# Performance work log

Measured on AMD Instinct MI355X. Metric: run time of the kernel, lower is better.

## Reference

```python
import jax, jax.numpy as jnp
import numpy as np


def _lstm_dir(xg, m, Whh, reverse):
    # xg: (T,B,4H) precomputed x@Wih.T + b ; m: (T,B) float mask
    T, B, G = xg.shape
    H = G // 4
    if reverse:
        xg = xg[::-1]
        m = m[::-1]

    def step(carry, inp):
        h, c = carry
        xg_t, m_t = inp
        gates = xg_t + h @ Whh.T
        i, f, g, o = jnp.split(gates, 4, axis=-1)  # torch gate order i,f,g,o
        i = jax.nn.sigmoid(i); f = jax.nn.sigmoid(f)
        g = jnp.tanh(g); o = jax.nn.sigmoid(o)
        c_new = f * c + i * g
        h_new = o * jnp.tanh(c_new)
        mt = m_t[:, None]
        h = mt * h_new + (1.0 - mt) * h
        c = mt * c_new + (1.0 - mt) * c
        return (h, c), h * mt  # zero outputs at padding like pad_packed_sequence

    init = (jnp.zeros((B, H), xg.dtype), jnp.zeros((B, H), xg.dtype))
    _, hs = jax.lax.scan(step, init, (xg, m))
    if reverse:
        hs = hs[::-1]
    return hs  # (T,B,H)


def _viterbi(feats, mask_f, transitions):
    # feats: (B,T,K) emissions incl. START/STOP rows; mask_f: (B,T) float
    B, T, K = feats.shape
    START, STOP = K - 2, K - 1
    part0 = transitions[START][None, :] + feats[:, 0, :]  # (B,K)
    ident = jnp.broadcast_to(jnp.arange(K)[None, :], (B, K))

    def step(part, inp):
        feat_t, m_t = inp
        cur = part[:, :, None] + transitions[None, :, :] + feat_t[:, None, :]
        new = cur.max(axis=1)
        bp = cur.argmax(axis=1)
        mb = (m_t > 0)[:, None]
        part = jnp.where(mb, new, part)        # carry partition through padding
        bp = jnp.where(mb, bp, ident)          # identity pointer at padding
        return part, bp

    part, bps = jax.lax.scan(
        step, part0, (feats[:, 1:].transpose(1, 0, 2), mask_f[:, 1:].T))
    final = part + transitions[:, STOP][None, :]
    best_score = final.max(axis=-1)            # (B,)
    last_tag = final.argmax(axis=-1)           # (B,)

    def back(tag, bp_t):
        prev = jnp.take_along_axis(bp_t, tag[:, None], axis=1)[:, 0]
        return prev, prev

    _, prevs = jax.lax.scan(back, last_tag, bps, reverse=True)  # (T-1,B)
    decode = jnp.concatenate([prevs, last_tag[None, :]], axis=0).T  # (B,T)
    return best_score, decode


def setup_inputs() -> dict:
    key = jax.random.key(0)
    ks = jax.random.split(key, 16)
    B, T, E, H = 256, 200, 256, 256
    Vc, Vf, n_labels = 10000, 100, 50
    K = n_labels + 2
    lengths = jnp.sort(jax.random.randint(ks[0], (B,), 1, T + 1))[::-1]
    lengths = lengths.at[0].set(T)
    mask = jnp.arange(T)[None, :] < lengths[:, None]
    s = 0.1
    trans = s * jax.random.normal(ks[11], (K, K), jnp.float32)
    trans = trans.at[:, K - 2].set(-10000.0)  # nothing transitions to START
    trans = trans.at[K - 1, :].set(-10000.0)  # nothing transitions from STOP
    return {
        'batch_input': jax.random.randint(ks[1], (B, T), 0, Vc),
        'batch_feature': jax.random.randint(ks[2], (B, T), 0, Vf),
        'batch_len': lengths,
        'batch_recover': jnp.arange(B),
        'mask': mask,
        'char_table': s * jax.random.normal(ks[3], (Vc, E), jnp.float32),
        'feat_table': 1.0 + s * jax.random.normal(ks[4], (Vf, E), jnp.float32),
        'Wih_f': s * jax.random.normal(ks[5], (4 * H, E), jnp.float32),
        'Whh_f': s * jax.random.normal(ks[6], (4 * H, H), jnp.float32),
        'b_f': s * jax.random.normal(ks[7], (4 * H,), jnp.float32),
        'Wih_b': s * jax.random.normal(ks[8], (4 * H, E), jnp.float32),
        'Whh_b': s * jax.random.normal(ks[9], (4 * H, H), jnp.float32),
        'b_b': s * jax.random.normal(ks[10], (4 * H,), jnp.float32),
        'W_tag': s * jax.random.normal(ks[12], (K, 2 * H), jnp.float32),
        'b_tag': s * jax.random.normal(ks[13], (K,), jnp.float32),
        'transitions': trans,
    }


def reference(batch_input, batch_feature, batch_len, batch_recover, mask,
              char_table, feat_table, Wih_f, Whh_f, b_f, Wih_b, Whh_b, b_b,
              W_tag, b_tag, transitions):
    # embeddings (dropout is identity at inference)
    emb = char_table[batch_input] * feat_table[batch_feature]  # (B,T,E)
    x = emb.transpose(1, 0, 2)                                 # (T,B,E)
    m = mask.astype(x.dtype).T                                 # (T,B)
    xg_f = jnp.einsum('tbe,ge->tbg', x, Wih_f) + b_f
    xg_b = jnp.einsum('tbe,ge->tbg', x, Wih_b) + b_b
    h_f = _lstm_dir(xg_f, m, Whh_f, reverse=False)
    h_b = _lstm_dir(xg_b, m, Whh_b, reverse=True)
    lstm_out = jnp.concatenate([h_f, h_b], axis=-1).transpose(1, 0, 2)  # (B,T,2H)
    feats = jnp.einsum('bth,kh->btk', lstm_out, W_tag) + b_tag          # (B,T,K)
    best_score, decode = _viterbi(feats, mask.astype(feats.dtype), transitions)
    decode = decode * mask.astype(decode.dtype)
    return best_score, decode
```

## Files before the change

kernel.cpp:

```cpp
#include <hip/hip_runtime.h>
#include <math.h>

#define T_ 200
#define WROW 284
#define SMEM_FLOATS (128 * WROW + 16 * WROW)
#define SMEM_BYTES (SMEM_FLOATS * 4)

typedef float f32x2 __attribute__((ext_vector_type(2)));

__device__ __forceinline__ float fsig(float x) {
  return 1.f / (1.f + __expf(-x));
}
__device__ __forceinline__ float ftanh(float x) {
  return 1.f - 2.f / (__expf(2.f * x) + 1.f);
}
__device__ __forceinline__ float dpp_xor1(float x) {
  return __int_as_float(__builtin_amdgcn_update_dpp(
      0, __float_as_int(x), 0xB1, 0xF, 0xF, true));
}
__device__ __forceinline__ float dpp_xor2(float x) {
  return __int_as_float(__builtin_amdgcn_update_dpp(
      0, __float_as_int(x), 0x4E, 0xF, 0xF, true));
}

__global__ __launch_bounds__(256) void xg_gemm(
    const int* __restrict__ bin, const int* __restrict__ bfe,
    const int* __restrict__ blen,
    const float* __restrict__ ctab, const float* __restrict__ ftab,
    const float* __restrict__ wihf, const float* __restrict__ biasf,
    const float* __restrict__ wihb, const float* __restrict__ biasb,
    float* __restrict__ xgf, float* __restrict__ xgb, int cc) {
  const int dir = blockIdx.z;
  const int m0 = blockIdx.x * 128;
  const int rloc = m0 >> 8;
  const int t_blk = dir ? (199 - cc - rloc) : (cc + rloc);
  if (t_blk >= blen[m0 & 255]) return;

  const float* wih  = dir ? wihb : wihf;
  const float* bias = dir ? biasb : biasf;
  float* xgslot     = dir ? xgb : xgf;

  __shared__ float As[32][140];
  __shared__ float Bs[32][132];
  const int tid = threadIdx.x;
  const int n0 = blockIdx.y * 128;
  const int mm = tid & 15;
  const int nn = tid >> 4;

  const int ra = tid & 127;
  const int ka = (tid >> 7) << 4;

  const int bcol = (m0 + ra) & 255;
  const float* cr = ctab + ((size_t)bin[bcol * T_ + t_blk] << 8);
  const float* fr = ftab + ((size_t)bfe[bcol * T_ + t_blk] << 8);
  const float* br = wih + (size_t)(n0 + ra) * 256;
  const int cwa = ra + ((ra >> 5) << 2);

  f32x2 acc[8][4];
  #pragma unroll
  for (int i = 0; i < 8; ++i)
    #pragma unroll
    for (int j = 0; j < 4; ++j) acc[i][j] = (f32x2){0.f, 0.f};

  const int am0 = mm * 8 + ((mm >> 2) << 2);
  const int bn0 = nn * 8;

  for (int ks = 0; ks < 256; ks += 32) {
    float4 c4[4], f4v[4], b4[4];
    #pragma unroll
    for (int w = 0; w < 4; ++w) {
      c4[w]  = *(const float4*)(cr + ks + ka + w * 4);
      f4v[w] = *(const float4*)(fr + ks + ka + w * 4);
      b4[w]  = *(const float4*)(br + ks + ka + w * 4);
    }
    __syncthreads();
    #pragma unroll
    for (int w = 0; w < 4; ++w) {
      int kk = ka + w * 4;
      As[kk + 0][cwa] = c4[w].x * f4v[w].x;
      As[kk + 1][cwa] = c4[w].y * f4v[w].y;
      As[kk + 2][cwa] = c4[w].z * f4v[w].z;
      As[kk + 3][cwa] = c4[w].w * f4v[w].w;
      Bs[kk + 0][ra] = b4[w].x;
      Bs[kk + 1][ra] = b4[w].y;
      Bs[kk + 2][ra] = b4[w].z;
      Bs[kk + 3][ra] = b4[w].w;
    }
    __syncthreads();
    #pragma unroll 4
    for (int k = 0; k < 32; ++k) {
      float4 a0 = *(const float4*)&As[k][am0];
      float4 a1 = *(const float4*)&As[k][am0 + 4];
      float4 b0 = *(const float4*)&Bs[k][bn0];
      float4 b1 = *(const float4*)&Bs[k][bn0 + 4];
      float am[8] = {a0.x, a0.y, a0.z, a0.w, a1.x, a1.y, a1.z, a1.w};
      f32x2 bp[4] = {{b0.x, b0.y}, {b0.z, b0.w}, {b1.x, b1.y}, {b1.z, b1.w}};
      #pragma unroll
      for (int i = 0; i < 8; ++i) {
        f32x2 av = {am[i], am[i]};
        #pragma unroll
        for (int j = 0; j < 4; ++j)
          acc[i][j] = __builtin_elementwise_fma(av, bp[j], acc[i][j]);
      }
    }
  }

  float4 bv0 = *(const float4*)(bias + n0 + bn0);
  float4 bv1 = *(const float4*)(bias + n0 + bn0 + 4);
  #pragma unroll
  for (int i = 0; i < 8; ++i) {
    int row = m0 + mm * 8 + i;
    float4 o0, o1;
    o0.x = acc[i][0].x + bv0.x; o0.y = acc[i][0].y + bv0.y;
    o0.z = acc[i][1].x + bv0.z; o0.w = acc[i][1].y + bv0.w;
    o1.x = acc[i][2].x + bv1.x; o1.y = acc[i][2].y + bv1.y;
    o1.z = acc[i][3].x + bv1.z; o1.w = acc[i][3].y + bv1.w;
    *(float4*)(xgslot + (size_t)row * 1024 + n0 + bn0) = o0;
    *(float4*)(xgslot + (size_t)row * 1024 + n0 + bn0 + 4) = o1;
  }
}

__global__ __launch_bounds__(512, 1) void lstm_chunk(
    const float* __restrict__ xgf, const float* __restrict__ xgb,
    const float* __restrict__ whf, const float* __restrict__ whb,
    const int* __restrict__ blen,
    float* __restrict__ hst, float* __restrict__ cst,
    float* __restrict__ hout, unsigned* __restrict__ bar,
    int s0, int nsteps) {
  extern __shared__ float smem[];
  float* wlds = smem;
  float* hlds = smem + 128 * WROW;

  const int bc = blockIdx.x, js = blockIdx.y, dir = blockIdx.z;
  const int tid = threadIdx.x;
  const int ks = tid & 7;
  const int bg = (tid >> 3) & 3;
  const int rg = tid >> 5;
  const int grp = dir * 16 + bc;
  const float* wh = dir ? whb : whf;
  const float* xgp = dir ? xgb : xgf;

  #pragma unroll
  for (int i = 0; i < 16; ++i) {
    int f = tid + i * 512;
    int prow = f >> 6;
    int k = (f & 63) << 2;
    int g = (prow >> 1) & 3, u = prow & 1, rgs = prow >> 3;
    int jg = js * 32 + rgs * 2 + u;
    float4 v = *(const float4*)(wh + ((size_t)(g * 256 + jg)) * 256 + k);
    *(float4*)&wlds[prow * WROW + k + ((k >> 5) << 2)] = v;
  }

  const int bl_th = bg * 4 + (ks & 3);
  const int b_th = bc * 16 + bl_th;
  const int u_th = ks >> 2;
  const int jth = js * 32 + rg * 2 + u_th;
  const int cjth = jth + ((jth >> 5) << 2);
  const int len_th = blen[b_th];
  float c0 = cst[((size_t)dir * 256 + b_th) * 256 + jth];

  float xq[4];
  #pragma unroll
  for (int g = 0; g < 4; ++g)
    xq[g] = xgp[(size_t)b_th * 1024 + g * 256 + jth];

  float hprev = 0.f;

  __syncthreads();

  for (int r = 0; r < nsteps; ++r) {
    const int s = s0 + r;
    const int tt = dir ? (199 - s) : s;
    const int rslot = s & 1, wslot = 1 - rslot;

    const float* hsrc = hst + (((size_t)(rslot * 2 + dir)) * 256 + bc * 16) * 256;
    {
      const int f0 = tid, f1 = tid + 512;
      const int b0i = f0 >> 6, k0 = (f0 & 63) << 2;
      const int b1i = f1 >> 6, k1 = (f1 & 63) << 2;
      const float* p0 = hsrc + (b0i << 8) + k0;
      const float* p1 = hsrc + (b1i << 8) + k1;
      float4 v0, v1;
      asm volatile(
          "global_load_dwordx4 %0, %2, off sc1\n\t"
          "global_load_dwordx4 %1, %3, off sc1\n\t"
          "s_waitcnt vmcnt(0)"
          : "=&v"(v0), "=&v"(v1)
          : "v"(p0), "v"(p1)
          : "memory");
      *(float4*)&hlds[b0i * WROW + k0 + ((k0 >> 5) << 2)] = v0;
      *(float4*)&hlds[b1i * WROW + k1 + ((k1 >> 5) << 2)] = v1;
    }
    __syncthreads();

    if (r == 0) hprev = hlds[bl_th * WROW + cjth];

    float xqn[4];
    const int rn = (r + 1 < nsteps) ? (r + 1) : r;
    #pragma unroll
    for (int g = 0; g < 4; ++g)
      xqn[g] = xgp[((size_t)rn * 256 + b_th) * 1024 + g * 256 + jth];

    f32x2 acc2[8][4];
    #pragma unroll
    for (int i = 0; i < 8; ++i)
      #pragma unroll
      for (int bb = 0; bb < 4; ++bb) acc2[i][bb] = (f32x2){0.f, 0.f};

    float4 w4c[8];
    #pragma unroll
    for (int i = 0; i < 8; ++i)
      w4c[i] = *(const float4*)&wlds[(rg * 8 + i) * WROW + ks * 36];

    #pragma unroll
    for (int kq = 0; kq < 8; ++kq) {
      const int col = ks * 36 + kq * 4;
      float4 h4[4];
      #pragma unroll
      for (int bb = 0; bb < 4; ++bb)
        h4[bb] = *(const float4*)&hlds[(bg * 4 + bb) * WROW + col];
      float4 w4n[8];
      if (kq < 7) {
        #pragma unroll
        for (int i = 0; i < 8; ++i)
          w4n[i] = *(const float4*)&wlds[(rg * 8 + i) * WROW + col + 4];
      }
      f32x2 hlo[4], hhi[4];
      #pragma unroll
      for (int bb = 0; bb < 4; ++bb) {
        hlo[bb] = (f32x2){h4[bb].x, h4[bb].y};
        hhi[bb] = (f32x2){h4[bb].z, h4[bb].w};
      }
      #pragma unroll
      for (int i = 0; i < 8; ++i) {
        f32x2 wlo = (f32x2){w4c[i].x, w4c[i].y};
        f32x2 whi = (f32x2){w4c[i].z, w4c[i].w};
        #pragma unroll
        for (int bb = 0; bb < 4; ++bb) {
          acc2[i][bb] = __builtin_elementwise_fma(wlo, hlo[bb], acc2[i][bb]);
          acc2[i][bb] = __builtin_elementwise_fma(whi, hhi[bb], acc2[i][bb]);
        }
      }
      if (kq < 7) {
        #pragma unroll
        for (int i = 0; i < 8; ++i) w4c[i] = w4n[i];
      }
    }

    float acc[8][4];
    #pragma unroll
    for (int i = 0; i < 8; ++i)
      #pragma unroll
      for (int bb = 0; bb < 4; ++bb)
        acc[i][bb] = acc2[i][bb].x + acc2[i][bb].y;

    const int bit0 = ks & 1, bit1 = (ks >> 1) & 1;
    float fin[8];
    #pragma unroll
    for (int i = 0; i < 8; ++i) {
      float k0 = bit0 ? acc[i][1] : acc[i][0];
      float s0v = bit0 ? acc[i][0] : acc[i][1];
      float k1 = bit0 ? acc[i][3] : acc[i][2];
      float s1v = bit0 ? acc[i][2] : acc[i][3];
      float r0 = k0 + dpp_xor1(s0v);
      float r1 = k1 + dpp_xor1(s1v);
      float k2 = bit1 ? r1 : r0;
      float s2v = bit1 ? r0 : r1;
      float r2 = k2 + dpp_xor2(s2v);
      fin[i] = r2 + __shfl_xor(r2, 4);
    }

    float gi = fsig((u_th ? fin[1] : fin[0]) + xq[0]);
    float gf = fsig((u_th ? fin[3] : fin[2]) + xq[1]);
    float gg = ftanh((u_th ? fin[5] : fin[4]) + xq[2]);
    float go = fsig((u_th ? fin[7] : fin[6]) + xq[3]);
    float cn = gf * c0 + gi * gg;
    float hn = go * ftanh(cn);
    const bool mk = tt < len_th;
    if (mk) c0 = cn;
    float hsv = mk ? hn : hprev;
    hprev = hsv;
    __hip_atomic_store(
        hst + (((size_t)(wslot * 2 + dir)) * 256 + b_th) * 256 + jth,
        hsv, __ATOMIC_RELAXED, __HIP_MEMORY_SCOPE_AGENT);

    asm volatile("s_waitcnt vmcnt(0)" ::: "memory");
    __syncthreads();
    if (tid == 0)
      __hip_atomic_fetch_add(&bar[grp * 32], 1u, __ATOMIC_RELAXED,
                             __HIP_MEMORY_SCOPE_AGENT);
    hout[(((size_t)dir * 200 + tt) * 256 + b_th) * 256 + jth] = mk ? hn : 0.f;
    if (tid == 0) {
      const unsigned tgt = 8u * (unsigned)(s + 1);
      while (__hip_atomic_load(&bar[grp * 32], __ATOMIC_RELAXED,
                               __HIP_MEMORY_SCOPE_AGENT) < tgt) {}
    }
    __syncthreads();

    #pragma unroll
    for (int g = 0; g < 4; ++g) xq[g] = xqn[g];
  }

  cst[((size_t)dir * 256 + b_th) * 256 + jth] = c0;
}

__global__ __launch_bounds__(256) void feats_kernel(
    const float* __restrict__ h_out, const float* __restrict__ wtag,
    const float* __restrict__ btag, float* __restrict__ feats,
    const int* __restrict__ blen) {
  const int t = blockIdx.x, bc = blockIdx.y;
  if (t >= blen[bc * 32]) return;
  __shared__ float hcat[32][512];
  const int tid = threadIdx.x;
  const float* hf = h_out + (((size_t)0 * 200 + t) * 256 + bc * 32) * 256;
  const float* hb = h_out + (((size_t)1 * 200 + t) * 256 + bc * 32) * 256;
  for (int i = tid; i < 2048; i += 256) {
    int row = i >> 6, c4 = (i & 63) << 2;
    *(float4*)&hcat[row][c4] = *(const float4*)(hf + (size_t)row * 256 + c4);
    *(float4*)&hcat[row][256 + c4] = *(const float4*)(hb + (size_t)row * 256 + c4);
  }
  __syncthreads();
  const int kk = tid & 63;
  const int bg = tid >> 6;
  if (kk < 52) {
    f32x2 acc2[8];
    #pragma unroll
    for (int i = 0; i < 8; ++i) acc2[i] = (f32x2){0.f, 0.f};
    const float* wr = wtag + (size_t)kk * 512;
    for (int jq = 0; jq < 128; ++jq) {
      float4 wv = *(const float4*)(wr + jq * 4);
      f32x2 wlo = (f32x2){wv.x, wv.y};
      f32x2 whi = (f32x2){wv.z, wv.w};
      #pragma unroll
      for (int bi = 0; bi < 8; ++bi) {
        float4 hv = *(const float4*)&hcat[bg * 8 + bi][jq * 4];
        f32x2 hlo = (f32x2){hv.x, hv.y};
        f32x2 hhi = (f32x2){hv.z, hv.w};
        acc2[bi] = __builtin_elementwise_fma(wlo, hlo, acc2[bi]);
        acc2[bi] = __builtin_elementwise_fma(whi, hhi, acc2[bi]);
      }
    }
    float bv = btag[kk];
    #pragma unroll
    for (int bi = 0; bi < 8; ++bi)
      feats[(size_t)(bc * 32 + bg * 8 + bi) * 10400 + t * 52 + kk] =
          acc2[bi].x + acc2[bi].y + bv;
  }
}

__global__ __launch_bounds__(64) void viterbi_kernel(
    const float* __restrict__ feats, const float* __restrict__ trans,
    const int* __restrict__ blen, float* __restrict__ out) {
  __shared__ float flds[10400];
  __shared__ float pl[56];
  __shared__ unsigned char bp[199 * 52];

  const int b = blockIdx.x;
  const int lane = threadIdx.x;
  const int kk = (lane < 52) ? lane : 0;
  const float* fb = feats + (size_t)b * 10400;
  const int len = blen[b];

  const int nf4 = (len * 52 + 3) >> 2;
  for (int i = lane; i < nf4; i += 64)
    *(float4*)&flds[i * 4] = *(const float4*)(fb + i * 4);

  float trc[52];
  #pragma unroll
  for (int j = 0; j < 52; ++j) trc[j] = trans[j * 52 + kk];
  __syncthreads();

  float part = trans[50 * 52 + kk] + flds[kk];
  if (lane < 52) pl[lane] = part;

  for (int t = 1; t < len; ++t) {
    const float ftk = flds[t * 52 + kk];
    float pa[52];
    #pragma unroll
    for (int q = 0; q < 13; ++q) {
      float4 v = *(const float4*)&pl[q * 4];
      pa[q * 4 + 0] = v.x; pa[q * 4 + 1] = v.y;
      pa[q * 4 + 2] = v.z; pa[q * 4 + 3] = v.w;
    }
    float mv0 = -1e30f, mv1 = -1e30f, mv2 = -1e30f, mv3 = -1e30f;
    int mj0 = 0, mj1 = 13, mj2 = 26, mj3 = 39;
    #pragma unroll
    for (int q = 0; q < 13; ++q) {
      float c0v = (pa[q] + trc[q]) + ftk;
      if (c0v > mv0) { mv0 = c0v; mj0 = q; }
      float c1v = (pa[13 + q] + trc[13 + q]) + ftk;
      if (c1v > mv1) { mv1 = c1v; mj1 = 13 + q; }
      float c2v = (pa[26 + q] + trc[26 + q]) + ftk;
      if (c2v > mv2) { mv2 = c2v; mj2 = 26 + q; }
      float c3v = (pa[39 + q] + trc[39 + q]) + ftk;
      if (c3v > mv3) { mv3 = c3v; mj3 = 39 + q; }
    }
    float mv = mv0; int mj = mj0;
    if (mv1 > mv) { mv = mv1; mj = mj1; }
    if (mv2 > mv) { mv = mv2; mj = mj2; }
    if (mv3 > mv) { mv = mv3; mj = mj3; }
    if (lane < 52) {
      bp[(t - 1) * 52 + lane] = (unsigned char)mj;
      part = mv; pl[lane] = mv;
    }
  }

  float fin = (lane < 52) ? (part + trans[lane * 52 + 51]) : -1e30f;
  int bi = lane;
  #pragma unroll
  for (int off = 32; off; off >>= 1) {
    float ov = __shfl_down(fin, off);
    int oi = __shfl_down(bi, off);
    if (ov > fin || (ov == fin && oi < bi)) { fin = ov; bi = oi; }
  }
  if (lane == 0) {
    out[b] = fin;
    float* dec = out + 256 + (size_t)b * 200;
    for (int i = len; i < 200; ++i) dec[i] = 0.f;
    int tag = bi;
    dec[len - 1] = (float)tag;
    for (int i = len - 2; i >= 0; --i) {
      tag = bp[i * 52 + tag];
      dec[i] = (float)tag;
    }
  }
}

extern "C" void kernel_launch(void* const* d_in, const int* in_sizes, int n_in,
                              void* d_out, int out_size, void* d_ws, size_t ws_size,
                              hipStream_t stream) {
  const int*   bin  = (const int*)d_in[0];
  const int*   bfe  = (const int*)d_in[1];
  const int*   blen = (const int*)d_in[2];
  const float* ctab = (const float*)d_in[5];
  const float* ftab = (const float*)d_in[6];
  const float* wihf = (const float*)d_in[7];
  const float* whhf = (const float*)d_in[8];
  const float* bf   = (const float*)d_in[9];
  const float* wihb = (const float*)d_in[10];
  const float* whhb = (const float*)d_in[11];
  const float* bb   = (const float*)d_in[12];
  const float* wtag = (const float*)d_in[13];
  const float* btag = (const float*)d_in[14];
  const float* trn  = (const float*)d_in[15];

  (void)hipFuncSetAttribute(reinterpret_cast<const void*>(lstm_chunk),
                            hipFuncAttributeMaxDynamicSharedMemorySize,
                            SMEM_BYTES);

  const size_t FIXED_F = 29271040;
  size_t ws_f = ws_size / sizeof(float);
  int C = 1;
  const int cands[10] = {50, 40, 25, 20, 10, 8, 5, 4, 2, 1};
  for (int u = 0; u < 10; ++u) {
    if (FIXED_F + (size_t)2 * cands[u] * 262144 <= ws_f) { C = cands[u]; break; }
  }

  float* ws  = (float*)d_ws;
  float* xgf = ws;
  float* xgb = xgf + (size_t)C * 262144;
  float* hst = xgb + (size_t)C * 262144;
  float* cst = hst + 262144;
  float* hout = cst + 131072;
  float* fts  = hout + 26214400;
  unsigned* bar = (unsigned*)(fts + 2662400);
  float* out  = (float*)d_out;

  hipMemsetAsync(hst, 0, (size_t)(262144 + 131072) * sizeof(float), stream);
  hipMemsetAsync(bar, 0, 1024 * sizeof(unsigned), stream);

  const int nchunks = 200 / C;
  for (int c = 0; c < nchunks; ++c) {
    xg_gemm<<<dim3(2 * C, 8, 2), 256, 0, stream>>>(
        bin, bfe, blen, ctab, ftab, wihf, bf, wihb, bb, xgf, xgb, c * C);
    lstm_chunk<<<dim3(16, 8, 2), 512, SMEM_BYTES, stream>>>(
        xgf, xgb, whhf, whhb, blen, hst, cst, hout, bar, c * C, C);
  }
  feats_kernel<<<dim3(200, 8), 256, 0, stream>>>(hout, wtag, btag, fts, blen);
  viterbi_kernel<<<256, 64, 0, stream>>>(fts, trn, blen, out);
}
```

Baseline: 1.986 ms.

## Precompute embeddings once, enlarge chunk candidates, and drop W register prefetch

Adds a separate kernel that gathers char and feature embeddings and multiplies them once into a workspace buffer. Both GEMM directions then read that buffer instead of each doing two gathers and a multiply. The chunk-size candidates now include 100 and 200, which allows fewer launches when the workspace is large enough. The LSTM inner loop stops double-buffering W fragments in registers and reads them straight from LDS, trading register pressure for more LDS loads and more workspace.

```diff
diff --git a/kernel.cpp b/kernel.cpp
--- a/kernel.cpp
+++ b/kernel.cpp
@@ -23,10 +23,32 @@
       0, __float_as_int(x), 0x4E, 0xF, 0xF, true));
 }
 
-__global__ __launch_bounds__(256) void xg_gemm(
+__global__ __launch_bounds__(256) void emb_kernel(
     const int* __restrict__ bin, const int* __restrict__ bfe,
     const int* __restrict__ blen,
     const float* __restrict__ ctab, const float* __restrict__ ftab,
+    float* __restrict__ emb) {
+  const int t = blockIdx.x;
+  const int bc8 = blockIdx.y;
+  if (t >= blen[(bc8 >= 4) ? 128 : 0]) return;
+  const int tid = threadIdx.x;
+  for (int i = tid; i < 2048; i += 256) {
+    int row = i >> 6;
+    int c4 = (i & 63) << 2;
+    int b = bc8 * 32 + row;
+    const float* cr = ctab + ((size_t)bin[b * T_ + t] << 8);
+    const float* fr = ftab + ((size_t)bfe[b * T_ + t] << 8);
+    float4 cv = *(const float4*)(cr + c4);
+    float4 fv = *(const float4*)(fr + c4);
+    float4 o;
+    o.x = cv.x * fv.x; o.y = cv.y * fv.y;
+    o.z = cv.z * fv.z; o.w = cv.w * fv.w;
+    *(float4*)(emb + ((size_t)t * 256 + b) * 256 + c4) = o;
+  }
+}
+
+__global__ __launch_bounds__(256) void xg_gemm(
+    const int* __restrict__ blen, const float* __restrict__ emb,
     const float* __restrict__ wihf, const float* __restrict__ biasf,
     const float* __restrict__ wihb, const float* __restrict__ biasb,
     float* __restrict__ xgf, float* __restrict__ xgb, int cc) {
@@ -51,8 +73,7 @@
   const int ka = (tid >> 7) << 4;
 
   const int bcol = (m0 + ra) & 255;
-  const float* cr = ctab + ((size_t)bin[bcol * T_ + t_blk] << 8);
-  const float* fr = ftab + ((size_t)bfe[bcol * T_ + t_blk] << 8);
+  const float* cr = emb + ((size_t)t_blk * 256 + bcol) * 256;
   const float* br = wih + (size_t)(n0 + ra) * 256;
   const int cwa = ra + ((ra >> 5) << 2);
 
@@ -66,21 +87,20 @@
   const int bn0 = nn * 8;
 
   for (int ks = 0; ks < 256; ks += 32) {
-    float4 c4[4], f4v[4], b4[4];
+    float4 c4[4], b4[4];
     #pragma unroll
     for (int w = 0; w < 4; ++w) {
-      c4[w]  = *(const float4*)(cr + ks + ka + w * 4);
-      f4v[w] = *(const float4*)(fr + ks + ka + w * 4);
-      b4[w]  = *(const float4*)(br + ks + ka + w * 4);
+      c4[w] = *(const float4*)(cr + ks + ka + w * 4);
+      b4[w] = *(const float4*)(br + ks + ka + w * 4);
     }
     __syncthreads();
     #pragma unroll
     for (int w = 0; w < 4; ++w) {
       int kk = ka + w * 4;
-      As[kk + 0][cwa] = c4[w].x * f4v[w].x;
-      As[kk + 1][cwa] = c4[w].y * f4v[w].y;
-      As[kk + 2][cwa] = c4[w].z * f4v[w].z;
-      As[kk + 3][cwa] = c4[w].w * f4v[w].w;
+      As[kk + 0][cwa] = c4[w].x;
+      As[kk + 1][cwa] = c4[w].y;
+      As[kk + 2][cwa] = c4[w].z;
+      As[kk + 3][cwa] = c4[w].w;
       Bs[kk + 0][ra] = b4[w].x;
       Bs[kk + 1][ra] = b4[w].y;
       Bs[kk + 2][ra] = b4[w].z;
@@ -207,11 +227,6 @@
       #pragma unroll
       for (int bb = 0; bb < 4; ++bb) acc2[i][bb] = (f32x2){0.f, 0.f};
 
-    float4 w4c[8];
-    #pragma unroll
-    for (int i = 0; i < 8; ++i)
-      w4c[i] = *(const float4*)&wlds[(rg * 8 + i) * WROW + ks * 36];
-
     #pragma unroll
     for (int kq = 0; kq < 8; ++kq) {
       const int col = ks * 36 + kq * 4;
@@ -219,12 +234,6 @@
       #pragma unroll
       for (int bb = 0; bb < 4; ++bb)
         h4[bb] = *(const float4*)&hlds[(bg * 4 + bb) * WROW + col];
-      float4 w4n[8];
-      if (kq < 7) {
-        #pragma unroll
-        for (int i = 0; i < 8; ++i)
-          w4n[i] = *(const float4*)&wlds[(rg * 8 + i) * WROW + col + 4];
-      }
       f32x2 hlo[4], hhi[4];
       #pragma unroll
       for (int bb = 0; bb < 4; ++bb) {
@@ -233,17 +242,14 @@
       }
       #pragma unroll
       for (int i = 0; i < 8; ++i) {
-        f32x2 wlo = (f32x2){w4c[i].x, w4c[i].y};
-        f32x2 whi = (f32x2){w4c[i].z, w4c[i].w};
+        float4 w4 = *(const float4*)&wlds[(rg * 8 + i) * WROW + col];
+        f32x2 wlo = (f32x2){w4.x, w4.y};
+        f32x2 whi = (f32x2){w4.z, w4.w};
         #pragma unroll
         for (int bb = 0; bb < 4; ++bb) {
           acc2[i][bb] = __builtin_elementwise_fma(wlo, hlo[bb], acc2[i][bb]);
           acc2[i][bb] = __builtin_elementwise_fma(whi, hhi[bb], acc2[i][bb]);
         }
-      }
-      if (kq < 7) {
-        #pragma unroll
-        for (int i = 0; i < 8; ++i) w4c[i] = w4n[i];
       }
     }
 
@@ -449,11 +455,14 @@
                             SMEM_BYTES);
 
   const size_t FIXED_F = 29271040;
+  const size_t EMB_F   = 13107200;
   size_t ws_f = ws_size / sizeof(float);
   int C = 1;
-  const int cands[10] = {50, 40, 25, 20, 10, 8, 5, 4, 2, 1};
-  for (int u = 0; u < 10; ++u) {
-    if (FIXED_F + (size_t)2 * cands[u] * 262144 <= ws_f) { C = cands[u]; break; }
+  const int cands[12] = {200, 100, 50, 40, 25, 20, 10, 8, 5, 4, 2, 1};
+  for (int u = 0; u < 12; ++u) {
+    if (FIXED_F + EMB_F + (size_t)2 * cands[u] * 262144 <= ws_f) {
+      C = cands[u]; break;
+    }
   }
 
   float* ws  = (float*)d_ws;
@@ -464,15 +473,18 @@
   float* hout = cst + 131072;
   float* fts  = hout + 26214400;
   unsigned* bar = (unsigned*)(fts + 2662400);
+  float* emb  = (float*)(bar + 1024);
   float* out  = (float*)d_out;
 
   hipMemsetAsync(hst, 0, (size_t)(262144 + 131072) * sizeof(float), stream);
   hipMemsetAsync(bar, 0, 1024 * sizeof(unsigned), stream);
+
+  emb_kernel<<<dim3(200, 8), 256, 0, stream>>>(bin, bfe, blen, ctab, ftab, emb);
 
   const int nchunks = 200 / C;
   for (int c = 0; c < nchunks; ++c) {
     xg_gemm<<<dim3(2 * C, 8, 2), 256, 0, stream>>>(
-        bin, bfe, blen, ctab, ftab, wihf, bf, wihb, bb, xgf, xgb, c * C);
+        blen, emb, wihf, bf, wihb, bb, xgf, xgb, c * C);
     lstm_chunk<<<dim3(16, 8, 2), 512, SMEM_BYTES, stream>>>(
         xgf, xgb, whhf, whhb, blen, hst, cst, hout, bar, c * C, C);
   }
```

Result: faster. 1.944 ms (-2.1%).

## Fuse next-chunk input GEMM into LSTM launch with double-buffered gate inputs

Applied to the files above, without the earlier changes.

Merges the per-chunk input-projection GEMM for chunk c+1 into the same launch as the recurrent LSTM work for chunk c, using extra blocks and double-buffered xg workspaces so projection overlaps the recurrence and launches are halved. LSTM blocks now skip steps outside their batch group's valid length range, with barrier targets rebased. The register-prefetched Whh tile is replaced by direct LDS reads per kq, and feats zero-fills dead rows. Doubles the xg workspace, which can shrink the chunk size, and the extra GEMM blocks may compete with the persistent LSTM blocks for CUs and spin-barrier progress.

```diff
diff --git a/kernel.cpp b/kernel.cpp
--- a/kernel.cpp
+++ b/kernel.cpp
@@ -21,6 +21,89 @@
 __device__ __forceinline__ float dpp_xor2(float x) {
   return __int_as_float(__builtin_amdgcn_update_dpp(
       0, __float_as_int(x), 0x4E, 0xF, 0xF, true));
+}
+
+__device__ __forceinline__ void xg_tile(
+    float* As, float* Bs,
+    int tid,
+    int t_blk, int m0, int n0,
+    const int* __restrict__ bin, const int* __restrict__ bfe,
+    const float* __restrict__ ctab, const float* __restrict__ ftab,
+    const float* __restrict__ wih, const float* __restrict__ bias,
+    float* __restrict__ xgslot) {
+  const int mm = tid & 15;
+  const int nn = tid >> 4;
+  const int ra = tid & 127;
+  const int ka = (tid >> 7) << 4;
+
+  const int bcol = (m0 + ra) & 255;
+  const float* cr = ctab + ((size_t)bin[bcol * T_ + t_blk] << 8);
+  const float* fr = ftab + ((size_t)bfe[bcol * T_ + t_blk] << 8);
+  const float* br = wih + (size_t)(n0 + ra) * 256;
+  const int cwa = ra + ((ra >> 5) << 2);
+
+  f32x2 acc[8][4];
+  #pragma unroll
+  for (int i = 0; i < 8; ++i)
+    #pragma unroll
+    for (int j = 0; j < 4; ++j) acc[i][j] = (f32x2){0.f, 0.f};
+
+  const int am0 = mm * 8 + ((mm >> 2) << 2);
+  const int bn0 = nn * 8;
+
+  for (int ks = 0; ks < 256; ks += 32) {
+    float4 c4[4], f4v[4], b4[4];
+    #pragma unroll
+    for (int w = 0; w < 4; ++w) {
+      c4[w]  = *(const float4*)(cr + ks + ka + w * 4);
+      f4v[w] = *(const float4*)(fr + ks + ka + w * 4);
+      b4[w]  = *(const float4*)(br + ks + ka + w * 4);
+    }
+    __syncthreads();
+    #pragma unroll
+    for (int w = 0; w < 4; ++w) {
+      int kk = ka + w * 4;
+      As[(kk + 0) * 140 + cwa] = c4[w].x * f4v[w].x;
+      As[(kk + 1) * 140 + cwa] = c4[w].y * f4v[w].y;
+      As[(kk + 2) * 140 + cwa] = c4[w].z * f4v[w].z;
+      As[(kk + 3) * 140 + cwa] = c4[w].w * f4v[w].w;
+      Bs[(kk + 0) * 132 + ra] = b4[w].x;
+      Bs[(kk + 1) * 132 + ra] = b4[w].y;
+      Bs[(kk + 2) * 132 + ra] = b4[w].z;
+      Bs[(kk + 3) * 132 + ra] = b4[w].w;
+    }
+    __syncthreads();
+    #pragma unroll 4
+    for (int k = 0; k < 32; ++k) {
+      float4 a0 = *(const float4*)&As[k * 140 + am0];
+      float4 a1 = *(const float4*)&As[k * 140 + am0 + 4];
+      float4 b0 = *(const float4*)&Bs[k * 132 + bn0];
+      float4 b1 = *(const float4*)&Bs[k * 132 + bn0 + 4];
+      float am[8] = {a0.x, a0.y, a0.z, a0.w, a1.x, a1.y, a1.z, a1.w};
+      f32x2 bp[4] = {{b0.x, b0.y}, {b0.z, b0.w}, {b1.x, b1.y}, {b1.z, b1.w}};
+      #pragma unroll
+      for (int i = 0; i < 8; ++i) {
+        f32x2 av = {am[i], am[i]};
+        #pragma unroll
+        for (int j = 0; j < 4; ++j)
+          acc[i][j] = __builtin_elementwise_fma(av, bp[j], acc[i][j]);
+      }
+    }
+  }
+
+  float4 bv0 = *(const float4*)(bias + n0 + bn0);
+  float4 bv1 = *(const float4*)(bias + n0 + bn0 + 4);
+  #pragma unroll
+  for (int i = 0; i < 8; ++i) {
+    int row = m0 + mm * 8 + i;
+    float4 o0, o1;
+    o0.x = acc[i][0].x + bv0.x; o0.y = acc[i][0].y + bv0.y;
+    o0.z = acc[i][1].x + bv0.z; o0.w = acc[i][1].y + bv0.w;
+    o1.x = acc[i][2].x + bv1.x; o1.y = acc[i][2].y + bv1.y;
+    o1.z = acc[i][3].x + bv1.z; o1.w = acc[i][3].y + bv1.w;
+    *(float4*)(xgslot + (size_t)row * 1024 + n0 + bn0) = o0;
+    *(float4*)(xgslot + (size_t)row * 1024 + n0 + bn0 + 4) = o1;
+  }
 }
 
 __global__ __launch_bounds__(256) void xg_gemm(
@@ -35,110 +118,64 @@
   const int rloc = m0 >> 8;
   const int t_blk = dir ? (199 - cc - rloc) : (cc + rloc);
   if (t_blk >= blen[m0 & 255]) return;
-
-  const float* wih  = dir ? wihb : wihf;
-  const float* bias = dir ? biasb : biasf;
-  float* xgslot     = dir ? xgb : xgf;
-
-  __shared__ float As[32][140];
-  __shared__ float Bs[32][132];
-  const int tid = threadIdx.x;
-  const int n0 = blockIdx.y * 128;
-  const int mm = tid & 15;
-  const int nn = tid >> 4;
-
-  const int ra = tid & 127;
-  const int ka = (tid >> 7) << 4;
-
-  const int bcol = (m0 + ra) & 255;
-  const float* cr = ctab + ((size_t)bin[bcol * T_ + t_blk] << 8);
-  const float* fr = ftab + ((size_t)bfe[bcol * T_ + t_blk] << 8);
-  const float* br = wih + (size_t)(n0 + ra) * 256;
-  const int cwa = ra + ((ra >> 5) << 2);
-
-  f32x2 acc[8][4];
-  #pragma unroll
-  for (int i = 0; i < 8; ++i)
-    #pragma unroll
-    for (int j = 0; j < 4; ++j) acc[i][j] = (f32x2){0.f, 0.f};
-
-  const int am0 = mm * 8 + ((mm >> 2) << 2);
-  const int bn0 = nn * 8;
-
-  for (int ks = 0; ks < 256; ks += 32) {
-    float4 c4[4], f4v[4], b4[4];
-    #pragma unroll
-    for (int w = 0; w < 4; ++w) {
-      c4[w]  = *(const float4*)(cr + ks + ka + w * 4);
-      f4v[w] = *(const float4*)(fr + ks + ka + w * 4);
-      b4[w]  = *(const float4*)(br + ks + ka + w * 4);
-    }
-    __syncthreads();
-    #pragma unroll
-    for (int w = 0; w < 4; ++w) {
-      int kk = ka + w * 4;
-      As[kk + 0][cwa] = c4[w].x * f4v[w].x;
-      As[kk + 1][cwa] = c4[w].y * f4v[w].y;
-      As[kk + 2][cwa] = c4[w].z * f4v[w].z;
-      As[kk + 3][cwa] = c4[w].w * f4v[w].w;
-      Bs[kk + 0][ra] = b4[w].x;
-      Bs[kk + 1][ra] = b4[w].y;
-      Bs[kk + 2][ra] = b4[w].z;
-      Bs[kk + 3][ra] = b4[w].w;
-    }
-    __syncthreads();
-    #pragma unroll 4
-    for (int k = 0; k < 32; ++k) {
-      float4 a0 = *(const float4*)&As[k][am0];
-      float4 a1 = *(const float4*)&As[k][am0 + 4];
-      float4 b0 = *(const float4*)&Bs[k][bn0];
-      float4 b1 = *(const float4*)&Bs[k][bn0 + 4];
-      float am[8] = {a0.x, a0.y, a0.z, a0.w, a1.x, a1.y, a1.z, a1.w};
-      f32x2 bp[4] = {{b0.x, b0.y}, {b0.z, b0.w}, {b1.x, b1.y}, {b1.z, b1.w}};
-      #pragma unroll
-      for (int i = 0; i < 8; ++i) {
-        f32x2 av = {am[i], am[i]};
-        #pragma unroll
-        for (int j = 0; j < 4; ++j)
-          acc[i][j] = __builtin_elementwise_fma(av, bp[j], acc[i][j]);
-      }
-    }
-  }
-
-  float4 bv0 = *(const float4*)(bias + n0 + bn0);
-  float4 bv1 = *(const float4*)(bias + n0 + bn0 + 4);
-  #pragma unroll
-  for (int i = 0; i < 8; ++i) {
-    int row = m0 + mm * 8 + i;
-    float4 o0, o1;
-    o0.x = acc[i][0].x + bv0.x; o0.y = acc[i][0].y + bv0.y;
-    o0.z = acc[i][1].x + bv0.z; o0.w = acc[i][1].y + bv0.w;
-    o1.x = acc[i][2].x + bv1.x; o1.y = acc[i][2].y + bv1.y;
-    o1.z = acc[i][3].x + bv1.z; o1.w = acc[i][3].y + bv1.w;
-    *(float4*)(xgslot + (size_t)row * 1024 + n0 + bn0) = o0;
-    *(float4*)(xgslot + (size_t)row * 1024 + n0 + bn0 + 4) = o1;
-  }
-}
-
-__global__ __launch_bounds__(512, 1) void lstm_chunk(
-    const float* __restrict__ xgf, const float* __restrict__ xgb,
+  __shared__ float As[32 * 140];
+  __shared__ float Bs[32 * 132];
+  xg_tile(As, Bs, threadIdx.x, t_blk, m0, blockIdx.y * 128, bin, bfe, ctab,
+          ftab, dir ? wihb : wihf, dir ? biasb : biasf, dir ? xgb : xgf);
+}
+
+__global__ __launch_bounds__(512, 1) void lstm_fused(
+    const float* __restrict__ xgfr, const float* __restrict__ xgbr,
     const float* __restrict__ whf, const float* __restrict__ whb,
     const int* __restrict__ blen,
     float* __restrict__ hst, float* __restrict__ cst,
     float* __restrict__ hout, unsigned* __restrict__ bar,
-    int s0, int nsteps) {
+    int s0, int nsteps, int Cn,
+    const int* __restrict__ bin, const int* __restrict__ bfe,
+    const float* __restrict__ ctab, const float* __restrict__ ftab,
+    const float* __restrict__ wihf, const float* __restrict__ biasf,
+    const float* __restrict__ wihb, const float* __restrict__ biasb,
+    float* __restrict__ xgfw, float* __restrict__ xgbw, int ccn) {
   extern __shared__ float smem[];
+  const int bid = blockIdx.x;
+
+  if (bid >= 256) {
+    const int xid = bid - 256;
+    const int x = xid % (2 * Cn);
+    const int rest = xid / (2 * Cn);
+    const int pair = rest & 3;
+    const int dirx = rest >> 2;
+    const int m0 = x * 128;
+    const int rloc = x >> 1;
+    const int t_blk = dirx ? (199 - ccn - rloc) : (ccn + rloc);
+    if (t_blk >= blen[(x & 1) * 128]) return;
+    const int half = threadIdx.x >> 8;
+    float* As = smem + half * 8704;
+    float* Bs = As + 32 * 140;
+    xg_tile(As, Bs, threadIdx.x & 255, t_blk, m0, (pair * 2 + half) * 128,
+            bin, bfe, ctab, ftab, dirx ? wihb : wihf, dirx ? biasb : biasf,
+            dirx ? xgbw : xgfw);
+    return;
+  }
+
   float* wlds = smem;
   float* hlds = smem + 128 * WROW;
 
-  const int bc = blockIdx.x, js = blockIdx.y, dir = blockIdx.z;
+  const int bc = bid & 15, js = (bid >> 4) & 7, dir = bid >> 7;
   const int tid = threadIdx.x;
   const int ks = tid & 7;
   const int bg = (tid >> 3) & 3;
   const int rg = tid >> 5;
   const int grp = dir * 16 + bc;
   const float* wh = dir ? whb : whf;
-  const float* xgp = dir ? xgb : xgf;
+  const float* xgp = dir ? xgbr : xgfr;
+
+  const int maxlen = blen[bc * 16];
+  const int first_s = dir ? (200 - maxlen) : 0;
+  const int last_s  = dir ? 200 : maxlen;
+  if (s0 >= last_s || s0 + nsteps <= first_s) return;
+  const int r_lo = (first_s > s0) ? (first_s - s0) : 0;
+  const int r_hi = (last_s - s0 < nsteps) ? (last_s - s0) : nsteps;
 
   #pragma unroll
   for (int i = 0; i < 16; ++i) {
@@ -162,13 +199,13 @@
   float xq[4];
   #pragma unroll
   for (int g = 0; g < 4; ++g)
-    xq[g] = xgp[(size_t)b_th * 1024 + g * 256 + jth];
+    xq[g] = xgp[((size_t)r_lo * 256 + b_th) * 1024 + g * 256 + jth];
 
   float hprev = 0.f;
 
   __syncthreads();
 
-  for (int r = 0; r < nsteps; ++r) {
+  for (int r = r_lo; r < r_hi; ++r) {
     const int s = s0 + r;
     const int tt = dir ? (199 - s) : s;
     const int rslot = s & 1, wslot = 1 - rslot;
@@ -193,10 +230,10 @@
     }
     __syncthreads();
 
-    if (r == 0) hprev = hlds[bl_th * WROW + cjth];
+    if (r == r_lo) hprev = hlds[bl_th * WROW + cjth];
 
     float xqn[4];
-    const int rn = (r + 1 < nsteps) ? (r + 1) : r;
+    const int rn = (r + 1 < r_hi) ? (r + 1) : r;
     #pragma unroll
     for (int g = 0; g < 4; ++g)
       xqn[g] = xgp[((size_t)rn * 256 + b_th) * 1024 + g * 256 + jth];
@@ -206,11 +243,6 @@
     for (int i = 0; i < 8; ++i)
       #pragma unroll
       for (int bb = 0; bb < 4; ++bb) acc2[i][bb] = (f32x2){0.f, 0.f};
-
-    float4 w4c[8];
-    #pragma unroll
-    for (int i = 0; i < 8; ++i)
-      w4c[i] = *(const float4*)&wlds[(rg * 8 + i) * WROW + ks * 36];
 
     #pragma unroll
     for (int kq = 0; kq < 8; ++kq) {
@@ -219,12 +251,6 @@
       #pragma unroll
       for (int bb = 0; bb < 4; ++bb)
         h4[bb] = *(const float4*)&hlds[(bg * 4 + bb) * WROW + col];
-      float4 w4n[8];
-      if (kq < 7) {
-        #pragma unroll
-        for (int i = 0; i < 8; ++i)
-          w4n[i] = *(const float4*)&wlds[(rg * 8 + i) * WROW + col + 4];
-      }
       f32x2 hlo[4], hhi[4];
       #pragma unroll
       for (int bb = 0; bb < 4; ++bb) {
@@ -233,17 +259,14 @@
       }
       #pragma unroll
       for (int i = 0; i < 8; ++i) {
-        f32x2 wlo = (f32x2){w4c[i].x, w4c[i].y};
-        f32x2 whi = (f32x2){w4c[i].z, w4c[i].w};
+        float4 w4 = *(const float4*)&wlds[(rg * 8 + i) * WROW + col];
+        f32x2 wlo = (f32x2){w4.x, w4.y};
+        f32x2 whi = (f32x2){w4.z, w4.w};
         #pragma unroll
         for (int bb = 0; bb < 4; ++bb) {
           acc2[i][bb] = __builtin_elementwise_fma(wlo, hlo[bb], acc2[i][bb]);
           acc2[i][bb] = __builtin_elementwise_fma(whi, hhi[bb], acc2[i][bb]);
         }
-      }
-      if (kq < 7) {
-        #pragma unroll
-        for (int i = 0; i < 8; ++i) w4c[i] = w4n[i];
       }
     }
 
@@ -291,7 +314,7 @@
                              __HIP_MEMORY_SCOPE_AGENT);
     hout[(((size_t)dir * 200 + tt) * 256 + b_th) * 256 + jth] = mk ? hn : 0.f;
     if (tid == 0) {
-      const unsigned tgt = 8u * (unsigned)(s + 1);
+      const unsigned tgt = 8u * (unsigned)(s - first_s + 1);
       while (__hip_atomic_load(&bar[grp * 32], __ATOMIC_RELAXED,
                                __HIP_MEMORY_SCOPE_AGENT) < tgt) {}
     }
@@ -314,10 +337,14 @@
   const int tid = threadIdx.x;
   const float* hf = h_out + (((size_t)0 * 200 + t) * 256 + bc * 32) * 256;
   const float* hb = h_out + (((size_t)1 * 200 + t) * 256 + bc * 32) * 256;
+  const float4 z4 = {0.f, 0.f, 0.f, 0.f};
   for (int i = tid; i < 2048; i += 256) {
     int row = i >> 6, c4 = (i & 63) << 2;
-    *(float4*)&hcat[row][c4] = *(const float4*)(hf + (size_t)row * 256 + c4);
-    *(float4*)&hcat[row][256 + c4] = *(const float4*)(hb + (size_t)row * 256 + c4);
+    bool live = t < blen[bc * 32 + row];
+    *(float4*)&hcat[row][c4] =
+        live ? *(const float4*)(hf + (size_t)row * 256 + c4) : z4;
+    *(float4*)&hcat[row][256 + c4] =
+        live ? *(const float4*)(hb + (size_t)row * 256 + c4) : z4;
   }
   __syncthreads();
   const int kk = tid & 63;
@@ -444,7 +471,7 @@
   const float* btag = (const float*)d_in[14];
   const float* trn  = (const float*)d_in[15];
 
-  (void)hipFuncSetAttribute(reinterpret_cast<const void*>(lstm_chunk),
+  (void)hipFuncSetAttribute(reinterpret_cast<const void*>(lstm_fused),
                             hipFuncAttributeMaxDynamicSharedMemorySize,
                             SMEM_BYTES);
 
@@ -453,14 +480,16 @@
   int C = 1;
   const int cands[10] = {50, 40, 25, 20, 10, 8, 5, 4, 2, 1};
   for (int u = 0; u < 10; ++u) {
-    if (FIXED_F + (size_t)2 * cands[u] * 262144 <= ws_f) { C = cands[u]; break; }
-  }
-
-  float* ws  = (float*)d_ws;
-  float* xgf = ws;
-  float* xgb = xgf + (size_t)C * 262144;
-  float* hst = xgb + (size_t)C * 262144;
-  float* cst = hst + 262144;
+    if (FIXED_F + (size_t)4 * cands[u] * 262144 <= ws_f) { C = cands[u]; break; }
+  }
+
+  float* ws   = (float*)d_ws;
+  float* xg0f = ws;
+  float* xg0b = xg0f + (size_t)C * 262144;
+  float* xg1f = xg0b + (size_t)C * 262144;
+  float* xg1b = xg1f + (size_t)C * 262144;
+  float* hst  = xg1b + (size_t)C * 262144;
+  float* cst  = hst + 262144;
   float* hout = cst + 131072;
   float* fts  = hout + 26214400;
   unsigned* bar = (unsigned*)(fts + 2662400);
@@ -470,11 +499,18 @@
   hipMemsetAsync(bar, 0, 1024 * sizeof(unsigned), stream);
 
   const int nchunks = 200 / C;
+  xg_gemm<<<dim3(2 * C, 8, 2), 256, 0, stream>>>(
+      bin, bfe, blen, ctab, ftab, wihf, bf, wihb, bb, xg0f, xg0b, 0);
+
   for (int c = 0; c < nchunks; ++c) {
-    xg_gemm<<<dim3(2 * C, 8, 2), 256, 0, stream>>>(
-        bin, bfe, blen, ctab, ftab, wihf, bf, wihb, bb, xgf, xgb, c * C);
-    lstm_chunk<<<dim3(16, 8, 2), 512, SMEM_BYTES, stream>>>(
-        xgf, xgb, whhf, whhb, blen, hst, cst, hout, bar, c * C, C);
+    const int nxg = (c + 1 < nchunks) ? 16 * C : 0;
+    float* rf = (c & 1) ? xg1f : xg0f;
+    float* rb = (c & 1) ? xg1b : xg0b;
+    float* wf = (c & 1) ? xg0f : xg1f;
+    float* wb = (c & 1) ? xg0b : xg1b;
+    lstm_fused<<<dim3(256 + nxg), 512, SMEM_BYTES, stream>>>(
+        rf, rb, whhf, whhb, blen, hst, cst, hout, bar, c * C, C, C,
+        bin, bfe, ctab, ftab, wihf, bf, wihb, bb, wf, wb, (c + 1) * C);
   }
   feats_kernel<<<dim3(200, 8), 256, 0, stream>>>(hout, wtag, btag, fts, blen);
   viterbi_kernel<<<256, 64, 0, stream>>>(fts, trn, blen, out);
```

Result: slower. 2.438 ms (+22.8%).
